# Performance work log

Hardware: AMD Instinct MI355X
Metric: run time of the kernel (lower is better)

## Reference

```python
import jax, jax.numpy as jnp
import numpy as np
import math

N_NODES = 100000
N_EDGES = 500000
HEADS = 8
IN_CH = 128          # dim(x) + dim(feats) = 64 + 64
OUT_CH = 128         # heads * 16
HEAD_DIM = OUT_CH // HEADS
MSG_DIM = 64
TIME_DIM = 64
EDGE_DIM = MSG_DIM + TIME_DIM


def setup_inputs() -> dict:
    key = jax.random.key(0)
    ks = jax.random.split(key, 16)
    p = lambda k, shp: (jax.random.normal(k, shp, dtype=jnp.float32) * 0.02)
    return {
        "feats": jax.random.normal(ks[0], (N_NODES, 64), dtype=jnp.float32),
        "x": jax.random.normal(ks[1], (N_NODES, 64), dtype=jnp.float32),
        "last_update": jax.random.uniform(ks[2], (N_NODES,), dtype=jnp.float32),
        "edge_index": jax.random.randint(ks[3], (2, N_EDGES), 0, N_NODES, dtype=jnp.int64),
        "t": jax.random.uniform(ks[4], (N_EDGES,), dtype=jnp.float32),
        "msg": jax.random.normal(ks[5], (N_EDGES, MSG_DIM), dtype=jnp.float32),
        # TimeEncoder: cos(Linear(1, TIME_DIM)(t))
        "time_w": p(ks[6], (TIME_DIM,)),
        "time_b": p(ks[7], (TIME_DIM,)),
        # TransformerConv params
        "Wq": p(ks[8], (IN_CH, OUT_CH)),
        "bq": jnp.zeros((OUT_CH,), jnp.float32),
        "Wk": p(ks[9], (IN_CH, OUT_CH)),
        "bk": jnp.zeros((OUT_CH,), jnp.float32),
        "Wv": p(ks[10], (IN_CH, OUT_CH)),
        "bv": jnp.zeros((OUT_CH,), jnp.float32),
        "We": p(ks[11], (EDGE_DIM, OUT_CH)),   # lin_edge, bias=False in PyG
        "Wskip": p(ks[12], (IN_CH, OUT_CH)),   # root weight skip connection
        "bskip": jnp.zeros((OUT_CH,), jnp.float32),
    }


def reference(feats, x, last_update, edge_index, t, msg,
              time_w, time_b, Wq, bq, Wk, bk, Wv, bv, We, Wskip, bskip):
    N = feats.shape[0]
    src, dst = edge_index[0], edge_index[1]  # message flows src -> dst

    # relative time encoding (TGN time encoder: cos(w*t + b))
    rel_t = last_update[src] - t                                  # [E]
    rel_t_enc = jnp.cos(rel_t[:, None] * time_w[None, :] + time_b)  # [E, TIME_DIM]
    edge_attr = jnp.concatenate([rel_t_enc, msg], axis=-1)        # [E, EDGE_DIM]

    h = jnp.concatenate([x, feats], axis=-1)                      # [N, IN_CH]

    q = (h @ Wq + bq).reshape(N, HEADS, HEAD_DIM)
    k = (h @ Wk + bk).reshape(N, HEADS, HEAD_DIM)
    v = (h @ Wv + bv).reshape(N, HEADS, HEAD_DIM)
    e = (edge_attr @ We).reshape(-1, HEADS, HEAD_DIM)             # [E, H, C]

    k_e = k[src] + e                                              # [E, H, C]
    alpha = jnp.sum(q[dst] * k_e, axis=-1) / math.sqrt(HEAD_DIM)  # [E, H]

    # segment softmax over incoming edges of each dst node
    m = jax.ops.segment_max(alpha, dst, num_segments=N)           # [N, H]
    m = jnp.where(jnp.isfinite(m), m, 0.0)
    ex = jnp.exp(alpha - m[dst])
    s = jax.ops.segment_sum(ex, dst, num_segments=N)              # [N, H]
    a = ex / (s[dst] + 1e-16)                                     # [E, H]

    out_e = (v[src] + e) * a[..., None]                           # [E, H, C]
    out = jax.ops.segment_sum(out_e, dst, num_segments=N)         # [N, H, C]
    out = out.reshape(N, HEADS * HEAD_DIM)
    return out + h @ Wskip + bskip
```

## Files before the change

### kernel.cpp

```cpp
#include <hip/hip_runtime.h>
#include <math.h>


typedef __attribute__((ext_vector_type(8))) short bf16x8;
typedef __attribute__((ext_vector_type(4))) float f32x4;

__device__ inline short f2bf(float f) {
  unsigned u = __float_as_uint(f);
  u += 0x7fff + ((u >> 16) & 1);
  return (short)(u >> 16);
}
__device__ inline float bf2f(short s) {
  return __uint_as_float(((unsigned)(unsigned short)s) << 16);
}
__device__ inline float bflo(unsigned u) { return __uint_as_float(u << 16); }
__device__ inline float bfhi(unsigned u) { return __uint_as_float(u & 0xffff0000u); }

__global__ void k_hist(const int* __restrict__ ei, int* __restrict__ counts, int E) {
  int i = blockIdx.x * 256 + threadIdx.x;
  if (i < E) atomicAdd(&counts[ei[E + i]], 1);
}

__global__ __launch_bounds__(1024) void k_bsum(const int* __restrict__ counts,
                                               int* __restrict__ bsum, int N) {
  int i = blockIdx.x * 1024 + threadIdx.x;
  int v = (i < N) ? counts[i] : 0;
  for (int d = 32; d; d >>= 1) v += __shfl_down(v, d);
  __shared__ int ws_[16];
  int lane = threadIdx.x & 63, wv = threadIdx.x >> 6;
  if (lane == 0) ws_[wv] = v;
  __syncthreads();
  if (threadIdx.x == 0) {
    int s = 0;
    for (int j = 0; j < 16; ++j) s += ws_[j];
    bsum[blockIdx.x] = s;
  }
}

__global__ __launch_bounds__(128) void k_bscan(const int* __restrict__ bsum,
                                               int* __restrict__ bpre, int nb) {
  __shared__ int sh[128];
  int t = threadIdx.x;
  sh[t] = (t < nb) ? bsum[t] : 0;
  __syncthreads();
  for (int d = 1; d < 128; d <<= 1) {
    int v = (t >= d) ? sh[t - d] : 0;
    __syncthreads();
    sh[t] += v;
    __syncthreads();
  }
  if (t < nb) bpre[t] = (t == 0) ? 0 : sh[t - 1];
}

__global__ __launch_bounds__(1024) void k_scan2(const int* __restrict__ counts,
                                                const int* __restrict__ bpre,
                                                int* __restrict__ offs,
                                                int* __restrict__ cursor, int N) {
  __shared__ int sh[1024];
  int t = threadIdx.x;
  int i = blockIdx.x * 1024 + t;
  int v = (i < N) ? counts[i] : 0;
  sh[t] = v;
  __syncthreads();
  for (int d = 1; d < 1024; d <<= 1) {
    int u = (t >= d) ? sh[t - d] : 0;
    __syncthreads();
    sh[t] += u;
    __syncthreads();
  }
  if (i < N) {
    int excl = bpre[blockIdx.x] + sh[t] - v;
    offs[i] = excl;
    cursor[i] = excl;
    if (i == N - 1) offs[N] = excl + v;
  }
}

__global__ void k_scatter(const int* __restrict__ ei, int* __restrict__ cursor,
                          int* __restrict__ rank, int* __restrict__ src_s, int E) {
  int i = blockIdx.x * 256 + threadIdx.x;
  if (i < E) {
    int pos = atomicAdd(&cursor[ei[E + i]], 1);
    rank[i] = pos;
    src_s[pos] = ei[i];
  }
}

struct PrepArgs { const float* W[5]; };
__global__ void k_prep(PrepArgs pa, short* __restrict__ wf) {
  int tid = blockIdx.x * 256 + threadIdx.x;
  if (tid >= 5 * 8 * 4 * 64) return;
  int lane = tid & 63;
  int kt = (tid >> 6) & 3;
  int nt = (tid >> 8) & 7;
  int mat = tid >> 11;
  const float* W = pa.W[mat];
  int n = nt * 16 + (lane & 15);
  short v[8];
#pragma unroll
  for (int j = 0; j < 8; ++j) {
    int k = kt * 32 + ((j >> 2) * 16) + ((lane >> 4) * 4) + (j & 3);
    v[j] = f2bf(W[k * 128 + n]);
  }
  ((uint4*)wf)[tid] = *(uint4*)v;
}

struct NodeArgs {
  const short* wf;
  const float* bias[4];
  void* outp[4];
};

__global__ __launch_bounds__(256, 2) void k_node(
    const float* __restrict__ x, const float* __restrict__ feats,
    NodeArgs na, int N) {
  __shared__ char lds[4][8192];
  const int lane = threadIdx.x & 63;
  const int wv = threadIdx.x >> 6;
  char* myl = lds[wv];

  bf16x8 bfrag[8][4];
  const uint4* wfp = (const uint4*)na.wf + (size_t)wv * 2048;
#pragma unroll
  for (int nt = 0; nt < 8; ++nt)
#pragma unroll
    for (int kt = 0; kt < 4; ++kt)
      *(uint4*)&bfrag[nt][kt] = wfp[(nt * 4 + kt) * 64 + lane];

  float biasv[8];
#pragma unroll
  for (int nt = 0; nt < 8; ++nt) biasv[nt] = na.bias[wv][nt * 16 + (lane & 15)];
  void* op = na.outp[wv];

  const int arow = lane & 15;
  const int k4 = (lane >> 4) * 4;
  const int ntiles = (N + 15) / 16;
  for (int tile = blockIdx.x; tile < ntiles; tile += gridDim.x) {
    int row = tile * 16 + arow;
    bool valid = row < N;
    const float* xr = x + (size_t)row * 64;
    const float* fr = feats + (size_t)row * 64;
    bf16x8 afrag[4];
#pragma unroll
    for (int kt = 0; kt < 4; ++kt) {
      const float* src = (kt < 2) ? xr : fr;
      int base = (kt & 1) * 32 + k4;
      float4 lo = valid ? *(const float4*)(src + base) : make_float4(0, 0, 0, 0);
      float4 hi = valid ? *(const float4*)(src + base + 16) : make_float4(0, 0, 0, 0);
      bf16x8 a;
      a[0] = f2bf(lo.x); a[1] = f2bf(lo.y); a[2] = f2bf(lo.z); a[3] = f2bf(lo.w);
      a[4] = f2bf(hi.x); a[5] = f2bf(hi.y); a[6] = f2bf(hi.z); a[7] = f2bf(hi.w);
      afrag[kt] = a;
    }
#pragma unroll
    for (int nt = 0; nt < 8; ++nt) {
      f32x4 acc = {0.f, 0.f, 0.f, 0.f};
#pragma unroll
      for (int kt = 0; kt < 4; ++kt)
        acc = __builtin_amdgcn_mfma_f32_16x16x32_bf16(afrag[kt], bfrag[nt][kt], acc, 0, 0, 0);
      int col = nt * 16 + (lane & 15);
#pragma unroll
      for (int reg = 0; reg < 4; ++reg) {
        int r = (lane >> 4) * 4 + reg;
        float vv = acc[reg] + biasv[nt];
        if (wv < 3) {
          int wb = (r * 256 + col * 2) ^ (((r >> 2) & 3) << 5);
          *(short*)(myl + wb) = f2bf(vv);
        } else {
          int wb = (r * 512 + col * 4) ^ (((r >> 2) & 3) << 6);
          *(float*)(myl + wb) = vv;
        }
      }
    }
    if (wv < 3) {
      short* opp = (short*)op;
#pragma unroll
      for (int i = 0; i < 8; ++i) {
        int r = i * 2 + (lane >> 5);
        int orow = tile * 16 + r;
        int rb = (r * 256 + (lane & 31) * 8) ^ (((r >> 2) & 3) << 5);
        uint2 val = *(const uint2*)(myl + rb);
        if (orow < N)
          *(uint2*)(opp + (size_t)orow * 128 + (lane & 31) * 4) = val;
      }
    } else {
      float* opp = (float*)op;
#pragma unroll
      for (int i = 0; i < 8; ++i) {
        int r = i * 2 + (lane >> 5);
        int orow = tile * 16 + r;
        int rb = (r * 512 + (lane & 31) * 16) ^ (((r >> 2) & 3) << 6);
        uint4 val = *(const uint4*)(myl + rb);
        if (orow < N)
          *(uint4*)(opp + (size_t)orow * 128 + (lane & 31) * 4) = val;
      }
    }
  }
}

__global__ __launch_bounds__(512) void k_egemm(
    const float* __restrict__ lu, const int* __restrict__ ei,
    const float* __restrict__ t, const float* __restrict__ msg,
    const float* __restrict__ tw, const float* __restrict__ tb,
    const short* __restrict__ wf, const int* __restrict__ rank,
    short* __restrict__ e_s, int E) {
  __shared__ uint4 wlds[2048];
  __shared__ char tbuf[8][4096];
  const int lane = threadIdx.x & 63;
  const int wv = threadIdx.x >> 6;
  char* myl = tbuf[wv];

  for (int i = threadIdx.x; i < 2048; i += 512)
    wlds[i] = ((const uint4*)wf)[8192 + i];
  __syncthreads();

  const int k4 = (lane >> 4) * 4;
  float twv[16], tbv[16];
#pragma unroll
  for (int kt = 0; kt < 2; ++kt) {
    int base = kt * 32 + k4;
    *(float4*)&twv[kt * 8]     = *(const float4*)(tw + base);
    *(float4*)&twv[kt * 8 + 4] = *(const float4*)(tw + base + 16);
    *(float4*)&tbv[kt * 8]     = *(const float4*)(tb + base);
    *(float4*)&tbv[kt * 8 + 4] = *(const float4*)(tb + base + 16);
  }

  const int ntiles = (E + 15) / 16;
  const int nwaves = gridDim.x * 8;
  int tile = blockIdx.x * 8 + wv;
  int p_src = 0, p_rank = 0;
  float p_t = 0.f;
  if (tile < ntiles && lane < 16 && tile * 16 + lane < E) {
    p_src  = ei[tile * 16 + lane];
    p_rank = rank[tile * 16 + lane];
    p_t    = t[tile * 16 + lane];
  }
  for (; tile < ntiles; tile += nwaves) {
    const int e0 = tile * 16;
    const int rank16 = p_rank;
    float relt = 0.f;
    if (lane < 16 && e0 + lane < E)
      relt = lu[p_src] - p_t;
    const int ntile = tile + nwaves;
    if (ntile < ntiles && lane < 16 && ntile * 16 + lane < E) {
      p_src  = ei[ntile * 16 + lane];
      p_rank = rank[ntile * 16 + lane];
      p_t    = t[ntile * 16 + lane];
    }
    const int r = lane & 15;
    float my_relt = __shfl(relt, r);
    bool rvalid = (e0 + r) < E;

    bf16x8 afrag[4];
#pragma unroll
    for (int kt = 0; kt < 2; ++kt) {
      bf16x8 a;
#pragma unroll
      for (int j = 0; j < 8; ++j)
        a[j] = f2bf(__cosf(my_relt * twv[kt * 8 + j] + tbv[kt * 8 + j]));
      afrag[kt] = a;
    }
    const float* mr = msg + (size_t)(e0 + r) * 64;
#pragma unroll
    for (int kt = 2; kt < 4; ++kt) {
      int base = (kt - 2) * 32 + k4;
      float4 lo = rvalid ? *(const float4*)(mr + base) : make_float4(0, 0, 0, 0);
      float4 hi = rvalid ? *(const float4*)(mr + base + 16) : make_float4(0, 0, 0, 0);
      bf16x8 a;
      a[0] = f2bf(lo.x); a[1] = f2bf(lo.y); a[2] = f2bf(lo.z); a[3] = f2bf(lo.w);
      a[4] = f2bf(hi.x); a[5] = f2bf(hi.y); a[6] = f2bf(hi.z); a[7] = f2bf(hi.w);
      afrag[kt] = a;
    }

#pragma unroll
    for (int nt = 0; nt < 8; ++nt) {
      bf16x8 bfrag[4];
#pragma unroll
      for (int kt = 0; kt < 4; ++kt)
        *(uint4*)&bfrag[kt] = wlds[(nt * 4 + kt) * 64 + lane];
      f32x4 acc = {0.f, 0.f, 0.f, 0.f};
#pragma unroll
      for (int kt = 0; kt < 4; ++kt)
        acc = __builtin_amdgcn_mfma_f32_16x16x32_bf16(afrag[kt], bfrag[kt], acc, 0, 0, 0);
      int col = nt * 16 + (lane & 15);
#pragma unroll
      for (int reg = 0; reg < 4; ++reg) {
        int rr = (lane >> 4) * 4 + reg;
        int wb = (rr * 256 + col * 2) ^ (((rr >> 2) & 3) << 5);
        *(short*)(myl + wb) = f2bf(acc[reg]);
      }
    }
#pragma unroll
    for (int i = 0; i < 8; ++i) {
      int rr = i * 2 + (lane >> 5);
      int er = e0 + rr;
      int drow = __shfl(rank16, rr);
      int rb = (rr * 256 + (lane & 31) * 8) ^ (((rr >> 2) & 3) << 5);
      uint2 val = *(const uint2*)(myl + rb);
      if (er < E)
        *(uint2*)(e_s + (size_t)drow * 128 + (lane & 31) * 4) = val;
    }
  }
}

__global__ __launch_bounds__(256) void k_agg(
    const int* __restrict__ offs, const int* __restrict__ src_s,
    const short* __restrict__ e_s, const short* __restrict__ qb,
    const short* __restrict__ kb, const short* __restrict__ vb,
    float* __restrict__ out, int N) {
  __shared__ int lds_vo[4][64];
  const int wave = threadIdx.x >> 6;
  const int lane = threadIdx.x & 63;
  const int n0 = (blockIdx.x * 4 + wave) * 2;
  if (n0 >= N) return;
  const int c2 = lane * 2;
  const bool hasB = (n0 + 1) < N;

  const int offA = offs[n0];
  const int endA = offs[n0 + 1];
  const int endB = hasB ? offs[n0 + 2] : endA;
  const int offB = endA;
  unsigned qvA = *(const unsigned*)(qb + (size_t)n0 * 128 + c2);
  unsigned qvB = hasB ? *(const unsigned*)(qb + (size_t)(n0 + 1) * 128 + c2) : 0u;
  float2 oA = *(float2*)(out + (size_t)n0 * 128 + c2);
  float2 oB = hasB ? *(float2*)(out + (size_t)(n0 + 1) * 128 + c2)
                   : make_float2(0.f, 0.f);

  auto process = [&](int off, int end, unsigned qv, float2& o) {
    if (end <= off) return;
    const float q0 = bflo(qv) * 0.36067376f;
    const float q1 = bfhi(qv) * 0.36067376f;
    float s = 0.f, acc0 = 0.f, acc1 = 0.f;
    for (int c0 = off; c0 < end; c0 += 64) {
      const int cnt = min(64, end - c0);
      if (lane < cnt) lds_vo[wave][lane] = src_s[c0 + lane] * 128;
      const int lim = cnt - 1;
      for (int g0 = 0; g0 < cnt; g0 += 8) {
        unsigned evr[8], kvr[8], vvr[8];
#pragma unroll
        for (int g = 0; g < 8; ++g) {
          int jj = g0 + g;
          jj = (jj > lim) ? lim : jj;
          int vo = lds_vo[wave][jj];
          evr[g] = *(const unsigned*)(e_s + (size_t)(c0 + jj) * 128 + c2);
          kvr[g] = *(const unsigned*)(kb + vo + c2);
          vvr[g] = *(const unsigned*)(vb + vo + c2);
        }
#pragma unroll
        for (int g = 0; g < 8; ++g) {
          float part = q0 * (bflo(kvr[g]) + bflo(evr[g]))
                     + q1 * (bfhi(kvr[g]) + bfhi(evr[g]));
          part += __shfl_xor(part, 1);
          part += __shfl_xor(part, 2);
          part += __shfl_xor(part, 4);
          float p = (g0 + g <= lim) ? exp2f(part) : 0.f;
          s += p;
          acc0 = fmaf(p, bflo(vvr[g]) + bflo(evr[g]), acc0);
          acc1 = fmaf(p, bfhi(vvr[g]) + bfhi(evr[g]), acc1);
        }
      }
    }
    float r = 1.f / (s + 1e-16f);
    o.x += acc0 * r;
    o.y += acc1 * r;
  };

  process(offA, endA, qvA, oA);
  *(float2*)(out + (size_t)n0 * 128 + c2) = oA;
  if (hasB) {
    process(offB, endB, qvB, oB);
    *(float2*)(out + (size_t)(n0 + 1) * 128 + c2) = oB;
  }
}

extern "C" void kernel_launch(void* const* d_in, const int* in_sizes, int n_in,
                              void* d_out, int out_size, void* d_ws, size_t ws_size,
                              hipStream_t stream) {
  const float* feats = (const float*)d_in[0];
  const float* x     = (const float*)d_in[1];
  const float* lu    = (const float*)d_in[2];
  const int*   ei    = (const int*)d_in[3];
  const float* t     = (const float*)d_in[4];
  const float* msg   = (const float*)d_in[5];
  const float* tw    = (const float*)d_in[6];
  const float* tb    = (const float*)d_in[7];
  const float* Wq    = (const float*)d_in[8];
  const float* bq    = (const float*)d_in[9];
  const float* Wk    = (const float*)d_in[10];
  const float* bk    = (const float*)d_in[11];
  const float* Wv    = (const float*)d_in[12];
  const float* bv    = (const float*)d_in[13];
  const float* We    = (const float*)d_in[14];
  const float* Wskip = (const float*)d_in[15];
  const float* bskip = (const float*)d_in[16];
  float* out = (float*)d_out;
  const int N = in_sizes[2];
  const int E = in_sizes[4];

  char* ws = (char*)d_ws;
  short* wfrag = (short*)ws; ws += 5 * 2048 * 16;
  short* qb    = (short*)ws; ws += (size_t)N * 128 * 2;
  short* kbuf  = (short*)ws; ws += (size_t)N * 128 * 2;
  short* vbuf  = (short*)ws; ws += (size_t)N * 128 * 2;
  short* e_s   = (short*)ws; ws += (size_t)E * 128 * 2;
  int* counts  = (int*)ws;   ws += (size_t)(N + 1) * 4;
  int* offs    = (int*)ws;   ws += (size_t)(N + 4) * 4;
  int* cursor  = (int*)ws;   ws += (size_t)N * 4;
  int* rank    = (int*)ws;   ws += (size_t)E * 4;
  int* src_s   = (int*)ws;   ws += (size_t)E * 4;
  int* bsum    = (int*)ws;   ws += 128 * 4;
  int* bpre    = (int*)ws;   ws += 128 * 4;

  const int nb = (N + 1023) / 1024;

  hipMemsetAsync(counts, 0, (size_t)(N + 1) * 4, stream);
  k_hist<<<(E + 255) / 256, 256, 0, stream>>>(ei, counts, E);
  k_bsum<<<nb, 1024, 0, stream>>>(counts, bsum, N);
  k_bscan<<<1, 128, 0, stream>>>(bsum, bpre, nb);
  k_scan2<<<nb, 1024, 0, stream>>>(counts, bpre, offs, cursor, N);
  k_scatter<<<(E + 255) / 256, 256, 0, stream>>>(ei, cursor, rank, src_s, E);

  PrepArgs pa;
  pa.W[0] = Wq; pa.W[1] = Wk; pa.W[2] = Wv; pa.W[3] = Wskip; pa.W[4] = We;
  k_prep<<<40, 256, 0, stream>>>(pa, wfrag);

  NodeArgs na;
  na.wf = wfrag;
  na.bias[0] = bq; na.bias[1] = bk; na.bias[2] = bv; na.bias[3] = bskip;
  na.outp[0] = qb; na.outp[1] = kbuf; na.outp[2] = vbuf; na.outp[3] = out;
  k_node<<<768, 256, 0, stream>>>(x, feats, na, N);

  k_egemm<<<512, 512, 0, stream>>>(lu, ei, t, msg, tw, tb, wfrag,
                                   rank, e_s, E);
  k_agg<<<(N + 7) / 8, 256, 0, stream>>>(offs, src_s, e_s, qb, kbuf, vbuf,
                                         out, N);
}
```

Measured before the change: 282.0 us.

## Merge node and edge GEMM kernels and fold weight prep and scan stages

Weight-fragment prep is merged with the destination histogram into one launch. The separate block-prefix scan kernel is removed, and each scan block now reduces its own preceding block sums. The node projection GEMM and the edge-attribute GEMM run in a single interleaved launch so the two independent workloads can overlap on the GPU. The edge path drops from 512 to 256 threads per block, and the aggregation softmax switches from exp2f with a prescaled q to __expf with a 0.25 scale. This cuts launch count and serialization, at the cost of a larger shared-memory footprint and a changed occupancy balance.

```diff
diff --git a/kernel.cpp b/kernel.cpp
--- a/kernel.cpp
+++ b/kernel.cpp
@@ -10,15 +10,34 @@
   u += 0x7fff + ((u >> 16) & 1);
   return (short)(u >> 16);
 }
-__device__ inline float bf2f(short s) {
-  return __uint_as_float(((unsigned)(unsigned short)s) << 16);
-}
 __device__ inline float bflo(unsigned u) { return __uint_as_float(u << 16); }
 __device__ inline float bfhi(unsigned u) { return __uint_as_float(u & 0xffff0000u); }
 
-__global__ void k_hist(const int* __restrict__ ei, int* __restrict__ counts, int E) {
-  int i = blockIdx.x * 256 + threadIdx.x;
-  if (i < E) atomicAdd(&counts[ei[E + i]], 1);
+struct PrepArgs { const float* W[5]; };
+__global__ void k_front(PrepArgs pa, short* __restrict__ wf,
+                        const int* __restrict__ ei, int* __restrict__ counts,
+                        int E) {
+  const int b = blockIdx.x;
+  if (b < 40) {
+    int tid = b * 256 + threadIdx.x;
+    if (tid >= 5 * 8 * 4 * 64) return;
+    int lane = tid & 63;
+    int kt = (tid >> 6) & 3;
+    int nt = (tid >> 8) & 7;
+    int mat = tid >> 11;
+    const float* W = pa.W[mat];
+    int n = nt * 16 + (lane & 15);
+    short v[8];
+#pragma unroll
+    for (int j = 0; j < 8; ++j) {
+      int k = kt * 32 + ((j >> 2) * 16) + ((lane >> 4) * 4) + (j & 3);
+      v[j] = f2bf(W[k * 128 + n]);
+    }
+    ((uint4*)wf)[tid] = *(uint4*)v;
+  } else {
+    int i = (b - 40) * 256 + threadIdx.x;
+    if (i < E) atomicAdd(&counts[ei[E + i]], 1);
+  }
 }
 
 __global__ __launch_bounds__(1024) void k_bsum(const int* __restrict__ counts,
@@ -37,28 +56,28 @@
   }
 }
 
-__global__ __launch_bounds__(128) void k_bscan(const int* __restrict__ bsum,
-                                               int* __restrict__ bpre, int nb) {
-  __shared__ int sh[128];
-  int t = threadIdx.x;
-  sh[t] = (t < nb) ? bsum[t] : 0;
+__global__ __launch_bounds__(1024) void k_scan2(const int* __restrict__ counts,
+                                                const int* __restrict__ bsum,
+                                                int* __restrict__ offs,
+                                                int* __restrict__ cursor,
+                                                int N, int nb) {
+  __shared__ int sh[1024];
+  __shared__ int wsum[16];
+  const int t = threadIdx.x;
+  const int b = blockIdx.x;
+  int pv = (t < b && t < nb) ? bsum[t] : 0;
+  for (int d = 32; d; d >>= 1) pv += __shfl_down(pv, d);
+  if ((t & 63) == 0) wsum[t >> 6] = pv;
   __syncthreads();
-  for (int d = 1; d < 128; d <<= 1) {
-    int v = (t >= d) ? sh[t - d] : 0;
-    __syncthreads();
-    sh[t] += v;
-    __syncthreads();
-  }
-  if (t < nb) bpre[t] = (t == 0) ? 0 : sh[t - 1];
-}
-
-__global__ __launch_bounds__(1024) void k_scan2(const int* __restrict__ counts,
-                                                const int* __restrict__ bpre,
-                                                int* __restrict__ offs,
-                                                int* __restrict__ cursor, int N) {
-  __shared__ int sh[1024];
-  int t = threadIdx.x;
-  int i = blockIdx.x * 1024 + t;
+  if (t == 0) {
+    int s = 0;
+    for (int j = 0; j < 16; ++j) s += wsum[j];
+    wsum[0] = s;
+  }
+  __syncthreads();
+  const int bpre = wsum[0];
+
+  int i = b * 1024 + t;
   int v = (i < N) ? counts[i] : 0;
   sh[t] = v;
   __syncthreads();
@@ -69,7 +88,7 @@
     __syncthreads();
   }
   if (i < N) {
-    int excl = bpre[blockIdx.x] + sh[t] - v;
+    int excl = bpre + sh[t] - v;
     offs[i] = excl;
     cursor[i] = excl;
     if (i == N - 1) offs[N] = excl + v;
@@ -86,219 +105,206 @@
   }
 }
 
-struct PrepArgs { const float* W[5]; };
-__global__ void k_prep(PrepArgs pa, short* __restrict__ wf) {
-  int tid = blockIdx.x * 256 + threadIdx.x;
-  if (tid >= 5 * 8 * 4 * 64) return;
-  int lane = tid & 63;
-  int kt = (tid >> 6) & 3;
-  int nt = (tid >> 8) & 7;
-  int mat = tid >> 11;
-  const float* W = pa.W[mat];
-  int n = nt * 16 + (lane & 15);
-  short v[8];
-#pragma unroll
-  for (int j = 0; j < 8; ++j) {
-    int k = kt * 32 + ((j >> 2) * 16) + ((lane >> 4) * 4) + (j & 3);
-    v[j] = f2bf(W[k * 128 + n]);
-  }
-  ((uint4*)wf)[tid] = *(uint4*)v;
-}
-
-struct NodeArgs {
+struct HeavyArgs {
   const short* wf;
   const float* bias[4];
   void* outp[4];
+  const float* lu;
+  const int* ei;
+  const float* t;
+  const float* msg;
+  const float* tw;
+  const float* tb;
+  const int* rank;
+  short* e_s;
 };
 
-__global__ __launch_bounds__(256, 2) void k_node(
+__global__ __launch_bounds__(256, 2) void k_heavy(
     const float* __restrict__ x, const float* __restrict__ feats,
-    NodeArgs na, int N) {
-  __shared__ char lds[4][8192];
+    HeavyArgs ha, int N, int E, int negemm, int nnode) {
+  __shared__ char smem[49152];
   const int lane = threadIdx.x & 63;
   const int wv = threadIdx.x >> 6;
-  char* myl = lds[wv];
-
-  bf16x8 bfrag[8][4];
-  const uint4* wfp = (const uint4*)na.wf + (size_t)wv * 2048;
-#pragma unroll
-  for (int nt = 0; nt < 8; ++nt)
-#pragma unroll
-    for (int kt = 0; kt < 4; ++kt)
-      *(uint4*)&bfrag[nt][kt] = wfp[(nt * 4 + kt) * 64 + lane];
-
-  float biasv[8];
-#pragma unroll
-  for (int nt = 0; nt < 8; ++nt) biasv[nt] = na.bias[wv][nt * 16 + (lane & 15)];
-  void* op = na.outp[wv];
-
-  const int arow = lane & 15;
-  const int k4 = (lane >> 4) * 4;
-  const int ntiles = (N + 15) / 16;
-  for (int tile = blockIdx.x; tile < ntiles; tile += gridDim.x) {
-    int row = tile * 16 + arow;
-    bool valid = row < N;
-    const float* xr = x + (size_t)row * 64;
-    const float* fr = feats + (size_t)row * 64;
-    bf16x8 afrag[4];
-#pragma unroll
-    for (int kt = 0; kt < 4; ++kt) {
-      const float* src = (kt < 2) ? xr : fr;
-      int base = (kt & 1) * 32 + k4;
-      float4 lo = valid ? *(const float4*)(src + base) : make_float4(0, 0, 0, 0);
-      float4 hi = valid ? *(const float4*)(src + base + 16) : make_float4(0, 0, 0, 0);
-      bf16x8 a;
-      a[0] = f2bf(lo.x); a[1] = f2bf(lo.y); a[2] = f2bf(lo.z); a[3] = f2bf(lo.w);
-      a[4] = f2bf(hi.x); a[5] = f2bf(hi.y); a[6] = f2bf(hi.z); a[7] = f2bf(hi.w);
-      afrag[kt] = a;
-    }
-#pragma unroll
-    for (int nt = 0; nt < 8; ++nt) {
-      f32x4 acc = {0.f, 0.f, 0.f, 0.f};
+  const int g = blockIdx.x / 5, r5 = blockIdx.x % 5;
+
+  if (r5 < 2) {
+    const int eb = g * 2 + r5;
+    if (eb >= negemm) return;
+    uint4* wlds = (uint4*)smem;
+    char* myl = smem + 32768 + wv * 4096;
+    for (int i = threadIdx.x; i < 2048; i += 256)
+      wlds[i] = ((const uint4*)ha.wf)[8192 + i];
+    __syncthreads();
+
+    const int k4 = (lane >> 4) * 4;
+    float twv[16], tbv[16];
+#pragma unroll
+    for (int kt = 0; kt < 2; ++kt) {
+      int base = kt * 32 + k4;
+      *(float4*)&twv[kt * 8]     = *(const float4*)(ha.tw + base);
+      *(float4*)&twv[kt * 8 + 4] = *(const float4*)(ha.tw + base + 16);
+      *(float4*)&tbv[kt * 8]     = *(const float4*)(ha.tb + base);
+      *(float4*)&tbv[kt * 8 + 4] = *(const float4*)(ha.tb + base + 16);
+    }
+
+    const int ntiles = (E + 15) / 16;
+    const int nwaves = negemm * 4;
+    int tile = eb * 4 + wv;
+    int p_src = 0, p_rank = 0;
+    float p_t = 0.f;
+    if (tile < ntiles && lane < 16 && tile * 16 + lane < E) {
+      p_src  = ha.ei[tile * 16 + lane];
+      p_rank = ha.rank[tile * 16 + lane];
+      p_t    = ha.t[tile * 16 + lane];
+    }
+    for (; tile < ntiles; tile += nwaves) {
+      const int e0 = tile * 16;
+      const int rank16 = p_rank;
+      float relt = 0.f;
+      if (lane < 16 && e0 + lane < E)
+        relt = ha.lu[p_src] - p_t;
+      const int ntile = tile + nwaves;
+      if (ntile < ntiles && lane < 16 && ntile * 16 + lane < E) {
+        p_src  = ha.ei[ntile * 16 + lane];
+        p_rank = ha.rank[ntile * 16 + lane];
+        p_t    = ha.t[ntile * 16 + lane];
+      }
+      const int r = lane & 15;
+      float my_relt = __shfl(relt, r);
+      bool rvalid = (e0 + r) < E;
+
+      bf16x8 afrag[4];
+#pragma unroll
+      for (int kt = 0; kt < 2; ++kt) {
+        bf16x8 a;
+#pragma unroll
+        for (int j = 0; j < 8; ++j)
+          a[j] = f2bf(__cosf(my_relt * twv[kt * 8 + j] + tbv[kt * 8 + j]));
+        afrag[kt] = a;
+      }
+      const float* mr = ha.msg + (size_t)(e0 + r) * 64;
+#pragma unroll
+      for (int kt = 2; kt < 4; ++kt) {
+        int base = (kt - 2) * 32 + k4;
+        float4 lo = rvalid ? *(const float4*)(mr + base) : make_float4(0, 0, 0, 0);
+        float4 hi = rvalid ? *(const float4*)(mr + base + 16) : make_float4(0, 0, 0, 0);
+        bf16x8 a;
+        a[0] = f2bf(lo.x); a[1] = f2bf(lo.y); a[2] = f2bf(lo.z); a[3] = f2bf(lo.w);
+        a[4] = f2bf(hi.x); a[5] = f2bf(hi.y); a[6] = f2bf(hi.z); a[7] = f2bf(hi.w);
+        afrag[kt] = a;
+      }
+
+#pragma unroll
+      for (int nt = 0; nt < 8; ++nt) {
+        bf16x8 bfrag[4];
+#pragma unroll
+        for (int kt = 0; kt < 4; ++kt)
+          *(uint4*)&bfrag[kt] = wlds[(nt * 4 + kt) * 64 + lane];
+        f32x4 acc = {0.f, 0.f, 0.f, 0.f};
+#pragma unroll
+        for (int kt = 0; kt < 4; ++kt)
+          acc = __builtin_amdgcn_mfma_f32_16x16x32_bf16(afrag[kt], bfrag[kt], acc, 0, 0, 0);
+        int col = nt * 16 + (lane & 15);
+#pragma unroll
+        for (int reg = 0; reg < 4; ++reg) {
+          int rr = (lane >> 4) * 4 + reg;
+          int wb = (rr * 256 + col * 2) ^ (((rr >> 2) & 3) << 5);
+          *(short*)(myl + wb) = f2bf(acc[reg]);
+        }
+      }
+#pragma unroll
+      for (int i = 0; i < 8; ++i) {
+        int rr = i * 2 + (lane >> 5);
+        int er = e0 + rr;
+        int drow = __shfl(rank16, rr);
+        int rb = (rr * 256 + (lane & 31) * 8) ^ (((rr >> 2) & 3) << 5);
+        uint2 val = *(const uint2*)(myl + rb);
+        if (er < E)
+          *(uint2*)(ha.e_s + (size_t)drow * 128 + (lane & 31) * 4) = val;
+      }
+    }
+  } else {
+    const int nb2 = g * 3 + (r5 - 2);
+    if (nb2 >= nnode) return;
+    char* myl = smem + wv * 8192;
+
+    bf16x8 bfrag[8][4];
+    const uint4* wfp = (const uint4*)ha.wf + (size_t)wv * 2048;
+#pragma unroll
+    for (int nt = 0; nt < 8; ++nt)
 #pragma unroll
       for (int kt = 0; kt < 4; ++kt)
-        acc = __builtin_amdgcn_mfma_f32_16x16x32_bf16(afrag[kt], bfrag[nt][kt], acc, 0, 0, 0);
-      int col = nt * 16 + (lane & 15);
-#pragma unroll
-      for (int reg = 0; reg < 4; ++reg) {
-        int r = (lane >> 4) * 4 + reg;
-        float vv = acc[reg] + biasv[nt];
-        if (wv < 3) {
-          int wb = (r * 256 + col * 2) ^ (((r >> 2) & 3) << 5);
-          *(short*)(myl + wb) = f2bf(vv);
-        } else {
-          int wb = (r * 512 + col * 4) ^ (((r >> 2) & 3) << 6);
-          *(float*)(myl + wb) = vv;
-        }
-      }
-    }
-    if (wv < 3) {
-      short* opp = (short*)op;
-#pragma unroll
-      for (int i = 0; i < 8; ++i) {
-        int r = i * 2 + (lane >> 5);
-        int orow = tile * 16 + r;
-        int rb = (r * 256 + (lane & 31) * 8) ^ (((r >> 2) & 3) << 5);
-        uint2 val = *(const uint2*)(myl + rb);
-        if (orow < N)
-          *(uint2*)(opp + (size_t)orow * 128 + (lane & 31) * 4) = val;
-      }
-    } else {
-      float* opp = (float*)op;
-#pragma unroll
-      for (int i = 0; i < 8; ++i) {
-        int r = i * 2 + (lane >> 5);
-        int orow = tile * 16 + r;
-        int rb = (r * 512 + (lane & 31) * 16) ^ (((r >> 2) & 3) << 6);
-        uint4 val = *(const uint4*)(myl + rb);
-        if (orow < N)
-          *(uint4*)(opp + (size_t)orow * 128 + (lane & 31) * 4) = val;
-      }
-    }
-  }
-}
-
-__global__ __launch_bounds__(512) void k_egemm(
-    const float* __restrict__ lu, const int* __restrict__ ei,
-    const float* __restrict__ t, const float* __restrict__ msg,
-    const float* __restrict__ tw, const float* __restrict__ tb,
-    const short* __restrict__ wf, const int* __restrict__ rank,
-    short* __restrict__ e_s, int E) {
-  __shared__ uint4 wlds[2048];
-  __shared__ char tbuf[8][4096];
-  const int lane = threadIdx.x & 63;
-  const int wv = threadIdx.x >> 6;
-  char* myl = tbuf[wv];
-
-  for (int i = threadIdx.x; i < 2048; i += 512)
-    wlds[i] = ((const uint4*)wf)[8192 + i];
-  __syncthreads();
-
-  const int k4 = (lane >> 4) * 4;
-  float twv[16], tbv[16];
-#pragma unroll
-  for (int kt = 0; kt < 2; ++kt) {
-    int base = kt * 32 + k4;
-    *(float4*)&twv[kt * 8]     = *(const float4*)(tw + base);
-    *(float4*)&twv[kt * 8 + 4] = *(const float4*)(tw + base + 16);
-    *(float4*)&tbv[kt * 8]     = *(const float4*)(tb + base);
-    *(float4*)&tbv[kt * 8 + 4] = *(const float4*)(tb + base + 16);
-  }
-
-  const int ntiles = (E + 15) / 16;
-  const int nwaves = gridDim.x * 8;
-  int tile = blockIdx.x * 8 + wv;
-  int p_src = 0, p_rank = 0;
-  float p_t = 0.f;
-  if (tile < ntiles && lane < 16 && tile * 16 + lane < E) {
-    p_src  = ei[tile * 16 + lane];
-    p_rank = rank[tile * 16 + lane];
-    p_t    = t[tile * 16 + lane];
-  }
-  for (; tile < ntiles; tile += nwaves) {
-    const int e0 = tile * 16;
-    const int rank16 = p_rank;
-    float relt = 0.f;
-    if (lane < 16 && e0 + lane < E)
-      relt = lu[p_src] - p_t;
-    const int ntile = tile + nwaves;
-    if (ntile < ntiles && lane < 16 && ntile * 16 + lane < E) {
-      p_src  = ei[ntile * 16 + lane];
-      p_rank = rank[ntile * 16 + lane];
-      p_t    = t[ntile * 16 + lane];
-    }
-    const int r = lane & 15;
-    float my_relt = __shfl(relt, r);
-    bool rvalid = (e0 + r) < E;
-
-    bf16x8 afrag[4];
-#pragma unroll
-    for (int kt = 0; kt < 2; ++kt) {
-      bf16x8 a;
-#pragma unroll
-      for (int j = 0; j < 8; ++j)
-        a[j] = f2bf(__cosf(my_relt * twv[kt * 8 + j] + tbv[kt * 8 + j]));
-      afrag[kt] = a;
-    }
-    const float* mr = msg + (size_t)(e0 + r) * 64;
-#pragma unroll
-    for (int kt = 2; kt < 4; ++kt) {
-      int base = (kt - 2) * 32 + k4;
-      float4 lo = rvalid ? *(const float4*)(mr + base) : make_float4(0, 0, 0, 0);
-      float4 hi = rvalid ? *(const float4*)(mr + base + 16) : make_float4(0, 0, 0, 0);
-      bf16x8 a;
-      a[0] = f2bf(lo.x); a[1] = f2bf(lo.y); a[2] = f2bf(lo.z); a[3] = f2bf(lo.w);
-      a[4] = f2bf(hi.x); a[5] = f2bf(hi.y); a[6] = f2bf(hi.z); a[7] = f2bf(hi.w);
-      afrag[kt] = a;
-    }
-
-#pragma unroll
-    for (int nt = 0; nt < 8; ++nt) {
-      bf16x8 bfrag[4];
-#pragma unroll
-      for (int kt = 0; kt < 4; ++kt)
-        *(uint4*)&bfrag[kt] = wlds[(nt * 4 + kt) * 64 + lane];
-      f32x4 acc = {0.f, 0.f, 0.f, 0.f};
-#pragma unroll
-      for (int kt = 0; kt < 4; ++kt)
-        acc = __builtin_amdgcn_mfma_f32_16x16x32_bf16(afrag[kt], bfrag[kt], acc, 0, 0, 0);
-      int col = nt * 16 + (lane & 15);
-#pragma unroll
-      for (int reg = 0; reg < 4; ++reg) {
-        int rr = (lane >> 4) * 4 + reg;
-        int wb = (rr * 256 + col * 2) ^ (((rr >> 2) & 3) << 5);
-        *(short*)(myl + wb) = f2bf(acc[reg]);
-      }
-    }
-#pragma unroll
-    for (int i = 0; i < 8; ++i) {
-      int rr = i * 2 + (lane >> 5);
-      int er = e0 + rr;
-      int drow = __shfl(rank16, rr);
-      int rb = (rr * 256 + (lane & 31) * 8) ^ (((rr >> 2) & 3) << 5);
-      uint2 val = *(const uint2*)(myl + rb);
-      if (er < E)
-        *(uint2*)(e_s + (size_t)drow * 128 + (lane & 31) * 4) = val;
+        *(uint4*)&bfrag[nt][kt] = wfp[(nt * 4 + kt) * 64 + lane];
+
+    float biasv[8];
+#pragma unroll
+    for (int nt = 0; nt < 8; ++nt)
+      biasv[nt] = ha.bias[wv][nt * 16 + (lane & 15)];
+    void* op = ha.outp[wv];
+
+    const int arow = lane & 15;
+    const int k4 = (lane >> 4) * 4;
+    const int ntiles = (N + 15) / 16;
+    for (int tile = nb2; tile < ntiles; tile += nnode) {
+      int row = tile * 16 + arow;
+      bool valid = row < N;
+      const float* xr = x + (size_t)row * 64;
+      const float* fr = feats + (size_t)row * 64;
+      bf16x8 afrag[4];
+#pragma unroll
+      for (int kt = 0; kt < 4; ++kt) {
+        const float* src = (kt < 2) ? xr : fr;
+        int base = (kt & 1) * 32 + k4;
+        float4 lo = valid ? *(const float4*)(src + base) : make_float4(0, 0, 0, 0);
+        float4 hi = valid ? *(const float4*)(src + base + 16) : make_float4(0, 0, 0, 0);
+        bf16x8 a;
+        a[0] = f2bf(lo.x); a[1] = f2bf(lo.y); a[2] = f2bf(lo.z); a[3] = f2bf(lo.w);
+        a[4] = f2bf(hi.x); a[5] = f2bf(hi.y); a[6] = f2bf(hi.z); a[7] = f2bf(hi.w);
+        afrag[kt] = a;
+      }
+#pragma unroll
+      for (int nt = 0; nt < 8; ++nt) {
+        f32x4 acc = {0.f, 0.f, 0.f, 0.f};
+#pragma unroll
+        for (int kt = 0; kt < 4; ++kt)
+          acc = __builtin_amdgcn_mfma_f32_16x16x32_bf16(afrag[kt], bfrag[nt][kt], acc, 0, 0, 0);
+        int col = nt * 16 + (lane & 15);
+#pragma unroll
+        for (int reg = 0; reg < 4; ++reg) {
+          int r = (lane >> 4) * 4 + reg;
+          float vv = acc[reg] + biasv[nt];
+          if (wv < 3) {
+            int wb = (r * 256 + col * 2) ^ (((r >> 2) & 3) << 5);
+            *(short*)(myl + wb) = f2bf(vv);
+          } else {
+            int wb = (r * 512 + col * 4) ^ (((r >> 2) & 3) << 6);
+            *(float*)(myl + wb) = vv;
+          }
+        }
+      }
+      if (wv < 3) {
+        short* opp = (short*)op;
+#pragma unroll
+        for (int i = 0; i < 8; ++i) {
+          int r = i * 2 + (lane >> 5);
+          int orow = tile * 16 + r;
+          int rb = (r * 256 + (lane & 31) * 8) ^ (((r >> 2) & 3) << 5);
+          uint2 val = *(const uint2*)(myl + rb);
+          if (orow < N)
+            *(uint2*)(opp + (size_t)orow * 128 + (lane & 31) * 4) = val;
+        }
+      } else {
+        float* opp = (float*)op;
+#pragma unroll
+        for (int i = 0; i < 8; ++i) {
+          int r = i * 2 + (lane >> 5);
+          int orow = tile * 16 + r;
+          int rb = (r * 512 + (lane & 31) * 16) ^ (((r >> 2) & 3) << 6);
+          uint4 val = *(const uint4*)(myl + rb);
+          if (orow < N)
+            *(uint4*)(opp + (size_t)orow * 128 + (lane & 31) * 4) = val;
+        }
+      }
     }
   }
 }
@@ -328,8 +334,7 @@
 
   auto process = [&](int off, int end, unsigned qv, float2& o) {
     if (end <= off) return;
-    const float q0 = bflo(qv) * 0.36067376f;
-    const float q1 = bfhi(qv) * 0.36067376f;
+    const float q0 = bflo(qv), q1 = bfhi(qv);
     float s = 0.f, acc0 = 0.f, acc1 = 0.f;
     for (int c0 = off; c0 < end; c0 += 64) {
       const int cnt = min(64, end - c0);
@@ -353,7 +358,7 @@
           part += __shfl_xor(part, 1);
           part += __shfl_xor(part, 2);
           part += __shfl_xor(part, 4);
-          float p = (g0 + g <= lim) ? exp2f(part) : 0.f;
+          float p = (g0 + g <= lim) ? __expf(part * 0.25f) : 0.f;
           s += p;
           acc0 = fmaf(p, bflo(vvr[g]) + bflo(evr[g]), acc0);
           acc1 = fmaf(p, bfhi(vvr[g]) + bfhi(evr[g]), acc1);
@@ -409,29 +414,29 @@
   int* rank    = (int*)ws;   ws += (size_t)E * 4;
   int* src_s   = (int*)ws;   ws += (size_t)E * 4;
   int* bsum    = (int*)ws;   ws += 128 * 4;
-  int* bpre    = (int*)ws;   ws += 128 * 4;
 
   const int nb = (N + 1023) / 1024;
+  const int nhist = (E + 255) / 256;
 
   hipMemsetAsync(counts, 0, (size_t)(N + 1) * 4, stream);
-  k_hist<<<(E + 255) / 256, 256, 0, stream>>>(ei, counts, E);
-  k_bsum<<<nb, 1024, 0, stream>>>(counts, bsum, N);
-  k_bscan<<<1, 128, 0, stream>>>(bsum, bpre, nb);
-  k_scan2<<<nb, 1024, 0, stream>>>(counts, bpre, offs, cursor, N);
-  k_scatter<<<(E + 255) / 256, 256, 0, stream>>>(ei, cursor, rank, src_s, E);
 
   PrepArgs pa;
   pa.W[0] = Wq; pa.W[1] = Wk; pa.W[2] = Wv; pa.W[3] = Wskip; pa.W[4] = We;
-  k_prep<<<40, 256, 0, stream>>>(pa, wfrag);
-
-  NodeArgs na;
-  na.wf = wfrag;
-  na.bias[0] = bq; na.bias[1] = bk; na.bias[2] = bv; na.bias[3] = bskip;
-  na.outp[0] = qb; na.outp[1] = kbuf; na.outp[2] = vbuf; na.outp[3] = out;
-  k_node<<<768, 256, 0, stream>>>(x, feats, na, N);
-
-  k_egemm<<<512, 512, 0, stream>>>(lu, ei, t, msg, tw, tb, wfrag,
-                                   rank, e_s, E);
+  k_front<<<40 + nhist, 256, 0, stream>>>(pa, wfrag, ei, counts, E);
+
+  k_bsum<<<nb, 1024, 0, stream>>>(counts, bsum, N);
+  k_scan2<<<nb, 1024, 0, stream>>>(counts, bsum, offs, cursor, N, nb);
+  k_scatter<<<nhist, 256, 0, stream>>>(ei, cursor, rank, src_s, E);
+
+  HeavyArgs ha;
+  ha.wf = wfrag;
+  ha.bias[0] = bq; ha.bias[1] = bk; ha.bias[2] = bv; ha.bias[3] = bskip;
+  ha.outp[0] = qb; ha.outp[1] = kbuf; ha.outp[2] = vbuf; ha.outp[3] = out;
+  ha.lu = lu; ha.ei = ei; ha.t = t; ha.msg = msg;
+  ha.tw = tw; ha.tb = tb; ha.rank = rank; ha.e_s = e_s;
+  const int negemm = 512, nnode = 768;
+  k_heavy<<<5 * 256, 256, 0, stream>>>(x, feats, ha, N, E, negemm, nnode);
+
   k_agg<<<(N + 7) / 8, 256, 0, stream>>>(offs, src_s, e_s, qb, kbuf, vbuf,
                                          out, N);
 }
```

Measured after the change: 300.7 us. 6.6% more time.
